# Kernel optimization log

Measured on AMD Instinct MI355X. Metric: run time of the kernel, lower is better.

## Reference

```python
import jax, jax.numpy as jnp
import numpy as np

N_EMBD = 1024
N_HEAD = 16
HEAD_DIM = N_EMBD // N_HEAD
NEG = -1e10


def setup_inputs() -> dict:
    key = jax.random.key(0)
    ks = jax.random.split(key, 5)
    B, T, C = 4, 2048, N_EMBD
    s = 0.02
    return {
        "x": jax.random.normal(ks[0], (B, T, C), dtype=jnp.float32),
        "w_attn": jax.random.normal(ks[1], (C, 3 * C), dtype=jnp.float32) * s,
        "b_attn": jnp.zeros((3 * C,), dtype=jnp.float32),
        "w_proj": jax.random.normal(ks[2], (C, C), dtype=jnp.float32) * s,
        "b_proj": jnp.zeros((C,), dtype=jnp.float32),
    }


def reference(x, w_attn, b_attn, w_proj, b_proj):
    B, T, C = x.shape
    H, D = N_HEAD, HEAD_DIM
    qkv = x @ w_attn + b_attn                      # [B,T,3C]
    q, k, v = jnp.split(qkv, 3, axis=-1)
    q = q.reshape(B, T, H, D).transpose(0, 2, 1, 3)  # [B,H,T,D]
    k = k.reshape(B, T, H, D).transpose(0, 2, 1, 3)
    v = v.reshape(B, T, H, D).transpose(0, 2, 1, 3)
    att = jnp.einsum("bhqd,bhkd->bhqk", q, k) / jnp.sqrt(jnp.float32(D))
    # additive causal mask: strictly-upper triangle gets -1e10 (as in torch source)
    mask = jnp.triu(jnp.full((T, T), NEG, dtype=att.dtype), k=1)
    att = jax.nn.softmax(att + mask, axis=-1)
    y = jnp.einsum("bhqk,bhkd->bhqd", att, v)      # [B,H,T,D]
    y = y.transpose(0, 2, 1, 3).reshape(B, T, C)
    return y @ w_proj + b_proj
```

## Files before the change

kernel.cpp:

```cpp
#include <hip/hip_runtime.h>
#include <hip/hip_bf16.h>

#define T_SEQ 2048
#define NE    1024
#define NH    16
#define HD    64
#define QKV_N 3072
#define MROWS 8192

typedef __attribute__((ext_vector_type(8))) short short8;
typedef __attribute__((ext_vector_type(4))) float f32x4;

__device__ __forceinline__ short f2bf(float f) {
  __hip_bfloat16 h = __float2bfloat16(f);
  return *reinterpret_cast<short*>(&h);
}
__device__ __forceinline__ float bfu2f(unsigned short u) {
  unsigned int t = (unsigned int)u << 16;
  return __builtin_bit_cast(float, t);
}

__device__ __forceinline__ void lds16(const void* g, void* l) {
  __builtin_amdgcn_global_load_lds(
      (const __attribute__((address_space(1))) unsigned int*)g,
      (__attribute__((address_space(3))) unsigned int*)l, 16, 0, 0);
}

__global__ __launch_bounds__(256) void cvt_bf16(const float* __restrict__ src,
                                                short* __restrict__ dst, int n8) {
  int i = blockIdx.x * 256 + threadIdx.x;
  const int stride = gridDim.x * 256;
  for (; i < n8; i += stride) {
    const float4* s = (const float4*)(src + (size_t)i * 8);
    float4 a = s[0], b = s[1];
    short8 v = short8{f2bf(a.x), f2bf(a.y), f2bf(a.z), f2bf(a.w),
                      f2bf(b.x), f2bf(b.y), f2bf(b.z), f2bf(b.w)};
    *(short8*)(dst + (size_t)i * 8) = v;
  }
}

__global__ __launch_bounds__(256) void transpose_cvt(const float* __restrict__ src,
                                                     short* __restrict__ dst,
                                                     int K, int N) {
  __shared__ short tile[32][33];
  int bn = blockIdx.x * 32;
  int bk = blockIdx.y * 32;
  int tx = threadIdx.x;
  int ty = threadIdx.y;
#pragma unroll
  for (int i = 0; i < 32; i += 8)
    tile[ty + i][tx] = f2bf(src[(size_t)(bk + ty + i) * N + bn + tx]);
  __syncthreads();
#pragma unroll
  for (int i = 0; i < 32; i += 8)
    dst[(size_t)(bn + ty + i) * K + bk + tx] = tile[tx][ty + i];
}

template <bool OUTF32>
__global__ __launch_bounds__(256) void gemm_bt_bias(const short* __restrict__ A,
                                                    const short* __restrict__ Bt,
                                                    const float* __restrict__ bias,
                                                    void* __restrict__ Co,
                                                    int M, int N, int K) {
  __shared__ __align__(16) short As[128 * 32];
  __shared__ __align__(16) short Bs[128 * 32];

  const int m0 = blockIdx.x * 128;
  const int n0 = blockIdx.y * 128;
  const int tid = threadIdx.x;
  const int w = tid >> 6, lane = tid & 63;
  const int L15 = lane & 15, quad = lane >> 4;
  const int wr = (w >> 1) * 64, wc = (w & 1) * 64;

  f32x4 acc[4][4] = {};

  for (int k0 = 0; k0 < K; k0 += 32) {
    __syncthreads();

#pragma unroll
    for (int p = 0; p < 2; ++p) {
      int r = p * 64 + w * 16 + (lane >> 2);
      int gl = (lane & 3) ^ ((r >> 1) & 3);
      lds16(A + (size_t)(m0 + r) * K + k0 + gl * 8, (char*)As + p * 4096 + w * 1024);
      lds16(Bt + (size_t)(n0 + r) * K + k0 + gl * 8, (char*)Bs + p * 4096 + w * 1024);
    }

    __syncthreads();

    short8 af[4], bfr[4];
#pragma unroll
    for (int i = 0; i < 4; ++i) {
      int r = wr + i * 16 + L15;
      af[i] = *(const short8*)(As + r * 32 + (quad ^ ((r >> 1) & 3)) * 8);
    }
#pragma unroll
    for (int j = 0; j < 4; ++j) {
      int r = wc + j * 16 + L15;
      bfr[j] = *(const short8*)(Bs + r * 32 + (quad ^ ((r >> 1) & 3)) * 8);
    }
#pragma unroll
    for (int i = 0; i < 4; ++i)
#pragma unroll
      for (int j = 0; j < 4; ++j)
        acc[i][j] = __builtin_amdgcn_mfma_f32_16x16x32_bf16(af[i], bfr[j], acc[i][j], 0, 0, 0);
  }

  float bv[4];
#pragma unroll
  for (int j = 0; j < 4; ++j) bv[j] = bias[n0 + wc + j * 16 + L15];
#pragma unroll
  for (int i = 0; i < 4; ++i)
#pragma unroll
    for (int j = 0; j < 4; ++j)
#pragma unroll
      for (int r = 0; r < 4; ++r) {
        size_t row = (size_t)(m0 + wr + i * 16 + quad * 4 + r);
        int col = n0 + wc + j * 16 + L15;
        float v = acc[i][j][r] + bv[j];
        if (OUTF32)
          ((float*)Co)[row * N + col] = v;
        else
          ((short*)Co)[row * N + col] = f2bf(v);
      }
}

__global__ __launch_bounds__(256) void attn_flash(const short* __restrict__ qkv,
                                                  short* __restrict__ y) {
  const int bx = blockIdx.x;
  const int bh = blockIdx.y;
  const int b = bh >> 4, h = bh & 15;
  const short* base = qkv + (size_t)b * T_SEQ * QKV_N;
  const int tid = threadIdx.x;
  const int w = tid >> 6, lane = tid & 63;
  const int L15 = lane & 15, quad = lane >> 4;

  __shared__ __align__(16) short Ks[64 * 80];
  __shared__ __align__(16) short Vts[64 * 80];
  __shared__ __align__(16) short Ps[4][32 * 72];

  const short one = (short)0x3F80;
  const short8 vone = short8{one, one, one, one, one, one, one, one};

  const float cs = 0.18033688011112042f;

  const short* kbase = base + NE + h * HD;
  const short* vbase = base + 2 * NE + h * HD;

  const int skey = tid >> 3;
  const int sd0 = (tid & 7) * 8;
  const int dv0 = w * 8;

#pragma unroll 1
  for (int seg = 0; seg < 2; ++seg) {
    const int qt = seg == 0 ? (T_SEQ / 128 - 1 - bx) : bx;

    short8 qf[2][2];
#pragma unroll
    for (int qs = 0; qs < 2; ++qs) {
      const short* qp =
          base + (size_t)(qt * 128 + w * 32 + qs * 16 + L15) * QKV_N + h * HD + quad * 8;
      qf[qs][0] = *(const short8*)qp;
      qf[qs][1] = *(const short8*)(qp + 32);
    }

    f32x4 O[2][4] = {};
    f32x4 L[2] = {};

    uint4 kv0 = *(const uint4*)(kbase + (size_t)skey * QKV_N + sd0);
    uint4 kv1 = *(const uint4*)(kbase + (size_t)(32 + skey) * QKV_N + sd0);
    uint4 vv0 = *(const uint4*)(vbase + (size_t)lane * QKV_N + dv0);
    uint4 vv1 = *(const uint4*)(vbase + (size_t)lane * QKV_N + dv0 + 32);

    const int nkt = 2 * qt + 2;
    for (int kt = 0; kt < nkt; ++kt) {
      __syncthreads();
      *(uint4*)&Ks[skey * 80 + sd0] = kv0;
      *(uint4*)&Ks[(32 + skey) * 80 + sd0] = kv1;
      {
        const short* pv0 = (const short*)&vv0;
        const short* pv1 = (const short*)&vv1;
#pragma unroll
        for (int j = 0; j < 8; ++j) {
          Vts[(dv0 + j) * 80 + lane] = pv0[j];
          Vts[(32 + dv0 + j) * 80 + lane] = pv1[j];
        }
      }
      __syncthreads();

      if (kt < nkt - 1) {
        int nt = kt + 1;
        kv0 = *(const uint4*)(kbase + (size_t)(nt * 64 + skey) * QKV_N + sd0);
        kv1 = *(const uint4*)(kbase + (size_t)(nt * 64 + 32 + skey) * QKV_N + sd0);
        vv0 = *(const uint4*)(vbase + (size_t)(nt * 64 + lane) * QKV_N + dv0);
        vv1 = *(const uint4*)(vbase + (size_t)(nt * 64 + lane) * QKV_N + dv0 + 32);
      }

      f32x4 S[2][4] = {};
#pragma unroll
      for (int nb = 0; nb < 4; ++nb) {
        short8 kb0 = *(const short8*)&Ks[(nb * 16 + L15) * 80 + quad * 8];
        short8 kb1 = *(const short8*)&Ks[(nb * 16 + L15) * 80 + 32 + quad * 8];
#pragma unroll
        for (int qs = 0; qs < 2; ++qs) {
          S[qs][nb] = __builtin_amdgcn_mfma_f32_16x16x32_bf16(qf[qs][0], kb0, S[qs][nb], 0, 0, 0);
          S[qs][nb] = __builtin_amdgcn_mfma_f32_16x16x32_bf16(qf[qs][1], kb1, S[qs][nb], 0, 0, 0);
        }
      }

      if (kt >= nkt - 2) {
#pragma unroll
        for (int qs = 0; qs < 2; ++qs)
#pragma unroll
          for (int nb = 0; nb < 4; ++nb) {
            int kg = kt * 64 + nb * 16 + L15;
#pragma unroll
            for (int r = 0; r < 4; ++r) {
              int qg = qt * 128 + w * 32 + qs * 16 + quad * 4 + r;
              if (kg > qg) S[qs][nb][r] = -1e30f;
            }
          }
      }

      short* myP = &Ps[w][0];
#pragma unroll
      for (int qs = 0; qs < 2; ++qs)
#pragma unroll
        for (int nb = 0; nb < 4; ++nb)
#pragma unroll
          for (int r = 0; r < 4; ++r)
            myP[(qs * 16 + quad * 4 + r) * 72 + nb * 16 + L15] =
                f2bf(__builtin_amdgcn_exp2f(S[qs][nb][r] * cs));
      asm volatile("" ::: "memory");
      short8 pf[2][2];
#pragma unroll
      for (int qs = 0; qs < 2; ++qs) {
        pf[qs][0] = *(const short8*)&myP[(qs * 16 + L15) * 72 + quad * 8];
        pf[qs][1] = *(const short8*)&myP[(qs * 16 + L15) * 72 + 32 + quad * 8];
      }

#pragma unroll
      for (int nb = 0; nb < 4; ++nb) {
        short8 vf0 = *(const short8*)&Vts[(nb * 16 + L15) * 80 + quad * 8];
        short8 vf1 = *(const short8*)&Vts[(nb * 16 + L15) * 80 + 32 + quad * 8];
#pragma unroll
        for (int qs = 0; qs < 2; ++qs) {
          O[qs][nb] = __builtin_amdgcn_mfma_f32_16x16x32_bf16(pf[qs][0], vf0, O[qs][nb], 0, 0, 0);
          O[qs][nb] = __builtin_amdgcn_mfma_f32_16x16x32_bf16(pf[qs][1], vf1, O[qs][nb], 0, 0, 0);
        }
      }
#pragma unroll
      for (int qs = 0; qs < 2; ++qs) {
        L[qs] = __builtin_amdgcn_mfma_f32_16x16x32_bf16(pf[qs][0], vone, L[qs], 0, 0, 0);
        L[qs] = __builtin_amdgcn_mfma_f32_16x16x32_bf16(pf[qs][1], vone, L[qs], 0, 0, 0);
      }
    }

#pragma unroll
    for (int qs = 0; qs < 2; ++qs) {
      float inv[4];
#pragma unroll
      for (int r = 0; r < 4; ++r) inv[r] = 1.0f / L[qs][r];
#pragma unroll
      for (int nb = 0; nb < 4; ++nb)
#pragma unroll
        for (int r = 0; r < 4; ++r) {
          size_t row =
              (size_t)b * T_SEQ + (size_t)(qt * 128 + w * 32 + qs * 16 + quad * 4 + r);
          int col = h * HD + nb * 16 + L15;
          y[row * NE + col] = f2bf(O[qs][nb][r] * inv[r]);
        }
    }
  }
}

extern "C" void kernel_launch(void* const* d_in, const int* in_sizes, int n_in,
                              void* d_out, int out_size, void* d_ws, size_t ws_size,
                              hipStream_t stream) {
  (void)in_sizes; (void)n_in; (void)out_size; (void)ws_size;
  const float* x      = (const float*)d_in[0];
  const float* w_attn = (const float*)d_in[1];
  const float* b_attn = (const float*)d_in[2];
  const float* w_proj = (const float*)d_in[3];
  const float* b_proj = (const float*)d_in[4];
  float* out = (float*)d_out;

  short* qkv = (short*)d_ws;
  short* wT2 = qkv;
  short* wT1 = qkv + (size_t)MROWS * QKV_N;
  short* y   = wT1;

  short* xb = (short*)d_out;

  cvt_bf16<<<2048, 256, 0, stream>>>(x, xb, MROWS * NE / 8);

  transpose_cvt<<<dim3(QKV_N / 32, NE / 32), dim3(32, 8), 0, stream>>>(w_attn, wT1, NE, QKV_N);

  gemm_bt_bias<false><<<dim3(MROWS / 128, QKV_N / 128), 256, 0, stream>>>(
      xb, wT1, b_attn, qkv, MROWS, QKV_N, NE);

  attn_flash<<<dim3(T_SEQ / 256, 64), 256, 0, stream>>>(qkv, y);

  transpose_cvt<<<dim3(NE / 32, NE / 32), dim3(32, 8), 0, stream>>>(w_proj, wT2, NE, NE);

  gemm_bt_bias<true><<<dim3(MROWS / 128, NE / 128), 256, 0, stream>>>(
      y, wT2, b_proj, out, MROWS, NE, NE);
}
```

Before: 265.5 us.

## Write V transposed from QKV GEMM and double-buffer K/V via direct LDS loads

The QKV GEMM epilogue now writes Q and K into a compact [M,2048] buffer and stores V already transposed per batch and head ([B*H*D, T]). This lets the attention kernel load K and V tiles straight into swizzled, double-buffered LDS with global_load_lds instead of staging them through registers and doing a scalar transpose. The aim is to cut the LDS transpose work and overlap the next tile's loads with compute, with one barrier per tile. The cost is a strided, poorly coalesced transposed store in the GEMM epilogue for the V columns.

```diff
diff --git a/kernel.cpp b/kernel.cpp
--- a/kernel.cpp
+++ b/kernel.cpp
@@ -6,6 +6,7 @@
 #define NH    16
 #define HD    64
 #define QKV_N 3072
+#define QK_N  2048
 #define MROWS 8192
 
 typedef __attribute__((ext_vector_type(8))) short short8;
@@ -14,10 +15,6 @@
 __device__ __forceinline__ short f2bf(float f) {
   __hip_bfloat16 h = __float2bfloat16(f);
   return *reinterpret_cast<short*>(&h);
-}
-__device__ __forceinline__ float bfu2f(unsigned short u) {
-  unsigned int t = (unsigned int)u << 16;
-  return __builtin_bit_cast(float, t);
 }
 
 __device__ __forceinline__ void lds16(const void* g, void* l) {
@@ -56,11 +53,12 @@
     dst[(size_t)(bn + ty + i) * K + bk + tx] = tile[tx][ty + i];
 }
 
-template <bool OUTF32>
+template <bool OUTF32, bool VSPLIT>
 __global__ __launch_bounds__(256) void gemm_bt_bias(const short* __restrict__ A,
                                                     const short* __restrict__ Bt,
                                                     const float* __restrict__ bias,
                                                     void* __restrict__ Co,
+                                                    short* __restrict__ Vt,
                                                     int M, int N, int K) {
   __shared__ __align__(16) short As[128 * 32];
   __shared__ __align__(16) short Bs[128 * 32];
@@ -108,34 +106,50 @@
   float bv[4];
 #pragma unroll
   for (int j = 0; j < 4; ++j) bv[j] = bias[n0 + wc + j * 16 + L15];
-#pragma unroll
-  for (int i = 0; i < 4; ++i)
-#pragma unroll
-    for (int j = 0; j < 4; ++j)
-#pragma unroll
-      for (int r = 0; r < 4; ++r) {
-        size_t row = (size_t)(m0 + wr + i * 16 + quad * 4 + r);
-        int col = n0 + wc + j * 16 + L15;
-        float v = acc[i][j][r] + bv[j];
-        if (OUTF32)
-          ((float*)Co)[row * N + col] = v;
-        else
-          ((short*)Co)[row * N + col] = f2bf(v);
-      }
-}
-
-__global__ __launch_bounds__(256) void attn_flash(const short* __restrict__ qkv,
+
+  if (VSPLIT && n0 >= 2 * NE) {
+#pragma unroll
+    for (int i = 0; i < 4; ++i)
+#pragma unroll
+      for (int j = 0; j < 4; ++j)
+#pragma unroll
+        for (int r = 0; r < 4; ++r) {
+          size_t row = (size_t)(m0 + wr + i * 16 + quad * 4 + r);
+          int col = n0 + wc + j * 16 + L15;
+          float v = acc[i][j][r] + bv[j];
+          Vt[(size_t)((row >> 11) * 1024 + (col - 2 * NE)) * T_SEQ + (row & 2047)] = f2bf(v);
+        }
+  } else {
+#pragma unroll
+    for (int i = 0; i < 4; ++i)
+#pragma unroll
+      for (int j = 0; j < 4; ++j)
+#pragma unroll
+        for (int r = 0; r < 4; ++r) {
+          size_t row = (size_t)(m0 + wr + i * 16 + quad * 4 + r);
+          int col = n0 + wc + j * 16 + L15;
+          float v = acc[i][j][r] + bv[j];
+          if (OUTF32)
+            ((float*)Co)[row * N + col] = v;
+          else
+            ((short*)Co)[row * (VSPLIT ? QK_N : N) + col] = f2bf(v);
+        }
+  }
+}
+
+__global__ __launch_bounds__(256) void attn_flash(const short* __restrict__ qk,
+                                                  const short* __restrict__ vt,
                                                   short* __restrict__ y) {
   const int bx = blockIdx.x;
   const int bh = blockIdx.y;
   const int b = bh >> 4, h = bh & 15;
-  const short* base = qkv + (size_t)b * T_SEQ * QKV_N;
+  const short* base = qk + (size_t)b * T_SEQ * QK_N;
   const int tid = threadIdx.x;
   const int w = tid >> 6, lane = tid & 63;
   const int L15 = lane & 15, quad = lane >> 4;
 
-  __shared__ __align__(16) short Ks[64 * 80];
-  __shared__ __align__(16) short Vts[64 * 80];
+  __shared__ __align__(16) short Ks[2][64 * 64];
+  __shared__ __align__(16) short Vs[2][64 * 64];
   __shared__ __align__(16) short Ps[4][32 * 72];
 
   const short one = (short)0x3F80;
@@ -143,12 +157,13 @@
 
   const float cs = 0.18033688011112042f;
 
-  const short* kbase = base + NE + h * HD;
-  const short* vbase = base + 2 * NE + h * HD;
-
-  const int skey = tid >> 3;
-  const int sd0 = (tid & 7) * 8;
-  const int dv0 = w * 8;
+  const short* kb_ = base + NE + h * HD;
+  const short* vb_ = vt + (size_t)bh * HD * T_SEQ;
+
+  const int srow = lane >> 3;
+  const int sg = lane & 7;
+
+  int cur = 0;
 
 #pragma unroll 1
   for (int seg = 0; seg < 2; ++seg) {
@@ -158,7 +173,7 @@
 #pragma unroll
     for (int qs = 0; qs < 2; ++qs) {
       const short* qp =
-          base + (size_t)(qt * 128 + w * 32 + qs * 16 + L15) * QKV_N + h * HD + quad * 8;
+          base + (size_t)(qt * 128 + w * 32 + qs * 16 + L15) * QK_N + h * HD + quad * 8;
       qf[qs][0] = *(const short8*)qp;
       qf[qs][1] = *(const short8*)(qp + 32);
     }
@@ -166,40 +181,38 @@
     f32x4 O[2][4] = {};
     f32x4 L[2] = {};
 
-    uint4 kv0 = *(const uint4*)(kbase + (size_t)skey * QKV_N + sd0);
-    uint4 kv1 = *(const uint4*)(kbase + (size_t)(32 + skey) * QKV_N + sd0);
-    uint4 vv0 = *(const uint4*)(vbase + (size_t)lane * QKV_N + dv0);
-    uint4 vv1 = *(const uint4*)(vbase + (size_t)lane * QKV_N + dv0 + 32);
-
     const int nkt = 2 * qt + 2;
+
+#pragma unroll
+    for (int p = 0; p < 2; ++p) {
+      int r = p * 32 + w * 8 + srow;
+      int gl = sg ^ (r & 7);
+      lds16(kb_ + (size_t)r * QK_N + gl * 8, (char*)&Ks[cur][0] + p * 4096 + w * 1024);
+      lds16(vb_ + (size_t)r * T_SEQ + gl * 8, (char*)&Vs[cur][0] + p * 4096 + w * 1024);
+    }
+    __syncthreads();
+
     for (int kt = 0; kt < nkt; ++kt) {
-      __syncthreads();
-      *(uint4*)&Ks[skey * 80 + sd0] = kv0;
-      *(uint4*)&Ks[(32 + skey) * 80 + sd0] = kv1;
-      {
-        const short* pv0 = (const short*)&vv0;
-        const short* pv1 = (const short*)&vv1;
-#pragma unroll
-        for (int j = 0; j < 8; ++j) {
-          Vts[(dv0 + j) * 80 + lane] = pv0[j];
-          Vts[(32 + dv0 + j) * 80 + lane] = pv1[j];
-        }
-      }
-      __syncthreads();
-
-      if (kt < nkt - 1) {
-        int nt = kt + 1;
-        kv0 = *(const uint4*)(kbase + (size_t)(nt * 64 + skey) * QKV_N + sd0);
-        kv1 = *(const uint4*)(kbase + (size_t)(nt * 64 + 32 + skey) * QKV_N + sd0);
-        vv0 = *(const uint4*)(vbase + (size_t)(nt * 64 + lane) * QKV_N + dv0);
-        vv1 = *(const uint4*)(vbase + (size_t)(nt * 64 + lane) * QKV_N + dv0 + 32);
-      }
+      if (kt + 1 < nkt) {
+#pragma unroll
+        for (int p = 0; p < 2; ++p) {
+          int r = p * 32 + w * 8 + srow;
+          int gl = sg ^ (r & 7);
+          lds16(kb_ + (size_t)((kt + 1) * 64 + r) * QK_N + gl * 8,
+                (char*)&Ks[cur ^ 1][0] + p * 4096 + w * 1024);
+          lds16(vb_ + (size_t)r * T_SEQ + (kt + 1) * 64 + gl * 8,
+                (char*)&Vs[cur ^ 1][0] + p * 4096 + w * 1024);
+        }
+      }
+      const short* K_ = &Ks[cur][0];
+      const short* V_ = &Vs[cur][0];
 
       f32x4 S[2][4] = {};
 #pragma unroll
       for (int nb = 0; nb < 4; ++nb) {
-        short8 kb0 = *(const short8*)&Ks[(nb * 16 + L15) * 80 + quad * 8];
-        short8 kb1 = *(const short8*)&Ks[(nb * 16 + L15) * 80 + 32 + quad * 8];
+        int r = nb * 16 + L15;
+        short8 kb0 = *(const short8*)&K_[r * 64 + ((quad ^ (r & 7)) * 8)];
+        short8 kb1 = *(const short8*)&K_[r * 64 + (((quad + 4) ^ (r & 7)) * 8)];
 #pragma unroll
         for (int qs = 0; qs < 2; ++qs) {
           S[qs][nb] = __builtin_amdgcn_mfma_f32_16x16x32_bf16(qf[qs][0], kb0, S[qs][nb], 0, 0, 0);
@@ -240,8 +253,9 @@
 
 #pragma unroll
       for (int nb = 0; nb < 4; ++nb) {
-        short8 vf0 = *(const short8*)&Vts[(nb * 16 + L15) * 80 + quad * 8];
-        short8 vf1 = *(const short8*)&Vts[(nb * 16 + L15) * 80 + 32 + quad * 8];
+        int r = nb * 16 + L15;
+        short8 vf0 = *(const short8*)&V_[r * 64 + ((quad ^ (r & 7)) * 8)];
+        short8 vf1 = *(const short8*)&V_[r * 64 + (((quad + 4) ^ (r & 7)) * 8)];
 #pragma unroll
         for (int qs = 0; qs < 2; ++qs) {
           O[qs][nb] = __builtin_amdgcn_mfma_f32_16x16x32_bf16(pf[qs][0], vf0, O[qs][nb], 0, 0, 0);
@@ -253,6 +267,9 @@
         L[qs] = __builtin_amdgcn_mfma_f32_16x16x32_bf16(pf[qs][0], vone, L[qs], 0, 0, 0);
         L[qs] = __builtin_amdgcn_mfma_f32_16x16x32_bf16(pf[qs][1], vone, L[qs], 0, 0, 0);
       }
+
+      __syncthreads();
+      cur ^= 1;
     }
 
 #pragma unroll
@@ -284,24 +301,24 @@
   const float* b_proj = (const float*)d_in[4];
   float* out = (float*)d_out;
 
-  short* qkv = (short*)d_ws;
-  short* wT2 = qkv;
-  short* wT1 = qkv + (size_t)MROWS * QKV_N;
+  short* qk  = (short*)d_ws;
+  short* vt  = qk + (size_t)MROWS * QK_N;
+  short* wT1 = vt + (size_t)NH * 4 * HD * T_SEQ;
   short* y   = wT1;
-
-  short* xb = (short*)d_out;
+  short* wT2 = qk;
+  short* xb  = (short*)d_out;
 
   cvt_bf16<<<2048, 256, 0, stream>>>(x, xb, MROWS * NE / 8);
 
   transpose_cvt<<<dim3(QKV_N / 32, NE / 32), dim3(32, 8), 0, stream>>>(w_attn, wT1, NE, QKV_N);
 
-  gemm_bt_bias<false><<<dim3(MROWS / 128, QKV_N / 128), 256, 0, stream>>>(
-      xb, wT1, b_attn, qkv, MROWS, QKV_N, NE);
-
-  attn_flash<<<dim3(T_SEQ / 256, 64), 256, 0, stream>>>(qkv, y);
+  gemm_bt_bias<false, true><<<dim3(MROWS / 128, QKV_N / 128), 256, 0, stream>>>(
+      xb, wT1, b_attn, qk, vt, MROWS, QKV_N, NE);
+
+  attn_flash<<<dim3(T_SEQ / 256, 64), 256, 0, stream>>>(qk, vt, y);
 
   transpose_cvt<<<dim3(NE / 32, NE / 32), dim3(32, 8), 0, stream>>>(w_proj, wT2, NE, NE);
 
-  gemm_bt_bias<true><<<dim3(MROWS / 128, NE / 128), 256, 0, stream>>>(
-      y, wT2, b_proj, out, MROWS, NE, NE);
-}
+  gemm_bt_bias<true, false><<<dim3(MROWS / 128, NE / 128), 256, 0, stream>>>(
+      y, wT2, b_proj, out, nullptr, MROWS, NE, NE);
+}
```

New measurement: 279.5 us. 5.3% more time.
